# Kernel optimization log

Hardware: AMD Instinct MI355X
Metric: run time of the kernel (lower is better)

## Reference

```python
import jax, jax.numpy as jnp
import numpy as np

B, S = 2, 2048
D, H, L = 768, 12, 2
DH = D // H
WIN = 128            # one-sided sliding window
C = WIN              # query chunk size
NC = S // C
FF = 4 * D
V = 50265
SEP_ID = 2
NSEP = 16
G = NSEP + 1         # CLS + all SEP tokens are global
NCLS = 7
HID = 100
NEG = -1e9
SEP_POS = np.arange(1, NSEP + 1) * 120   # fixed [SEP] layout, same every row


def setup_inputs() -> dict:
    key = jax.random.key(0)
    ks = iter(jax.random.split(key, 32))
    def p(shape, scale=0.02):
        return scale * jax.random.normal(next(ks), shape, jnp.float32)
    input_ids = jax.random.randint(next(ks), (B, S), 10, V)
    input_ids = input_ids.at[:, SEP_POS].set(SEP_ID)
    attention_mask = jnp.ones((B, S), jnp.int32)
    return dict(
        input_ids=input_ids, attention_mask=attention_mask,
        tok_emb=p((V, D)), pos_emb=p((S, D)),
        ln_e_g=jnp.ones((D,)), ln_e_b=jnp.zeros((D,)),
        Wq=p((L, D, D)), bq=jnp.zeros((L, D)),
        Wk=p((L, D, D)), bk=jnp.zeros((L, D)),
        Wv=p((L, D, D)), bv=jnp.zeros((L, D)),
        Wo=p((L, D, D)), bo=jnp.zeros((L, D)),
        ln1_g=jnp.ones((L, D)), ln1_b=jnp.zeros((L, D)),
        W1=p((L, D, FF)), b1=jnp.zeros((L, FF)),
        W2=p((L, FF, D)), b2=jnp.zeros((L, D)),
        ln2_g=jnp.ones((L, D)), ln2_b=jnp.zeros((L, D)),
        Wh=p((2 * D, HID)), bh=jnp.zeros((HID,)),
        Wout=p((HID, NCLS)), bout=jnp.zeros((NCLS,)),
    )


def _ln(x, g, b):
    mu = jnp.mean(x, -1, keepdims=True)
    var = jnp.var(x, -1, keepdims=True)
    return (x - mu) * jax.lax.rsqrt(var + 1e-5) * g + b


def forward(input_ids, attention_mask, tok_emb, pos_emb, ln_e_g, ln_e_b,
            Wq, bq, Wk, bk, Wv, bv, Wo, bo, ln1_g, ln1_b,
            W1, b1, W2, b2, ln2_g, ln2_b, Wh, bh, Wout, bout):
    # global positions: CLS + every [SEP] (same layout in every row)
    sep_pos = jnp.nonzero(input_ids[0] == SEP_ID, size=NSEP)[0]          # [NSEP]
    glob = jnp.concatenate([jnp.zeros((1,), sep_pos.dtype), sep_pos])    # [G]

    amask = attention_mask.astype(jnp.float32)                           # [B,S]
    is_glob = jnp.zeros((S,), bool).at[glob].set(True)

    # banded (sliding-window) gather pattern, padded-coordinate indices
    idx = jnp.arange(NC)[:, None] * C + jnp.arange(3 * C)[None, :]       # [NC,3C]
    pos_k = idx - C                                                      # abs key pos
    pos_q = jnp.arange(NC)[:, None] * C + jnp.arange(C)[None, :]         # [NC,C]
    pos_k_c = jnp.clip(pos_k, 0, S - 1)
    band = jnp.abs(pos_k[:, None, :] - pos_q[:, :, None]) <= WIN         # [NC,C,3C]
    inb = (pos_k >= 0) & (pos_k < S)                                     # [NC,3C]
    # global keys are handled by the dedicated global columns -> drop from band
    band = band & (inb & ~is_glob[pos_k_c])[:, None, :]
    km = amask[:, pos_k_c] * inb                                         # [B,NC,3C]
    valid = band[None] & (km[:, :, None, :] > 0)                         # [B,NC,C,3C]
    gmask = amask[:, glob] > 0                                           # [B,G]

    x = tok_emb[input_ids] + pos_emb[None]                               # [B,S,D]
    x = _ln(x, ln_e_g, ln_e_b)

    for l in range(L):
        q = (x @ Wq[l] + bq[l]).reshape(B, S, H, DH).transpose(0, 2, 1, 3) * (DH ** -0.5)
        k = (x @ Wk[l] + bk[l]).reshape(B, S, H, DH).transpose(0, 2, 1, 3)
        v = (x @ Wv[l] + bv[l]).reshape(B, S, H, DH).transpose(0, 2, 1, 3)
        kp = jnp.pad(k, ((0, 0), (0, 0), (C, C), (0, 0)))
        vp = jnp.pad(v, ((0, 0), (0, 0), (C, C), (0, 0)))
        k3 = kp[:, :, idx]                                               # [B,H,NC,3C,DH]
        v3 = vp[:, :, idx]
        qc = q.reshape(B, H, NC, C, DH)
        s_loc = jnp.einsum('bhncd,bhnkd->bhnck', qc, k3)                 # banded scores
        s_loc = jnp.where(valid[:, None], s_loc, NEG)
        kg, vg = k[:, :, glob], v[:, :, glob]                            # [B,H,G,DH]
        s_g = jnp.einsum('bhncd,bhgd->bhncg', qc, kg)
        s_g = jnp.where(gmask[:, None, None, None, :], s_g, NEG)
        p = jax.nn.softmax(jnp.concatenate([s_loc, s_g], axis=-1), axis=-1)
        out = (jnp.einsum('bhnck,bhnkd->bhncd', p[..., :3 * C], v3)
               + jnp.einsum('bhncg,bhgd->bhncd', p[..., 3 * C:], vg))
        out = out.reshape(B, H, S, DH)
        # global query rows attend to the full sequence
        qg = q[:, :, glob]
        s_full = jnp.einsum('bhgd,bhsd->bhgs', qg, k)
        s_full = jnp.where(amask[:, None, None, :] > 0, s_full, NEG)
        out_g = jnp.einsum('bhgs,bhsd->bhgd', jax.nn.softmax(s_full, -1), v)
        out = out.at[:, :, glob, :].set(out_g)
        a = out.transpose(0, 2, 1, 3).reshape(B, S, D) @ Wo[l] + bo[l]
        x = _ln(x + a, ln1_g[l], ln1_b[l])
        h = jax.nn.gelu(x @ W1[l] + b1[l])
        x = _ln(x + h @ W2[l] + b2[l], ln2_g[l], ln2_b[l])

    # core-sentence embeddings: hstack(CLS, interior SEP embeddings)
    core = sep_pos[1:-1]                                                 # [NSEP-2]
    cls = x[:, 0, :]                                                     # [B,D]
    seps = x[:, core, :]                                                 # [B,NSEP-2,D]
    emb = jnp.concatenate([jnp.broadcast_to(cls[:, None], seps.shape), seps], -1)
    emb = emb.reshape(B * (NSEP - 2), 2 * D)
    return jax.nn.relu(emb @ Wh + bh) @ Wout + bout                      # [28, NCLS]


def reference(input_ids, attention_mask, tok_emb, pos_emb, ln_e_g, ln_e_b,
              Wq, bq, Wk, bk, Wv, bv, Wo, bo, ln1_g, ln1_b,
              W1, b1, W2, b2, ln2_g, ln2_b, Wh, bh, Wout, bout):
    return forward(input_ids, attention_mask, tok_emb, pos_emb, ln_e_g, ln_e_b,
                   Wq, bq, Wk, bk, Wv, bv, Wo, bo, ln1_g, ln1_b,
                   W1, b1, W2, b2, ln2_g, ln2_b, Wh, bh, Wout, bout)
```

## Files before the change

kernel.cpp:

```cpp
#include <hip/hip_runtime.h>
#include <hip/hip_bf16.h>
#include <math.h>

#define Sdim 2048
#define Bdim 2
#define Ddim 768
#define Hdim 12
#define DHdim 64
#define Ldim 2
#define Cdim 128
#define NCdim 16
#define FFdim 3072
#define Gdim 17
#define NSEPd 16
#define HIDd 100
#define NCLSd 7
#define SEPID 2
#define MROWS (Bdim*Sdim)
#define QKVS 2304

typedef __bf16 bf16_t;
typedef bf16_t bf16x8 __attribute__((ext_vector_type(8)));
typedef float f32x4 __attribute__((ext_vector_type(4)));
typedef ushort ushort8v __attribute__((ext_vector_type(8)));

__device__ __forceinline__ ushort f2bf(float f) {
    union { float f; unsigned u; } a; a.f = f;
    unsigned u = a.u;
    unsigned r = (u + 0x7fffu + ((u >> 16) & 1u)) >> 16;
    return (ushort)r;
}
__device__ __forceinline__ float bf2f(ushort h) {
    union { unsigned u; float f; } a; a.u = ((unsigned)h) << 16;
    return a.f;
}
__device__ __forceinline__ void gload16(const ushort* g, ushort* l) {
    __builtin_amdgcn_global_load_lds(
        (const __attribute__((address_space(1))) void*)g,
        (__attribute__((address_space(3))) void*)l, 16, 0, 0);
}

__global__ __launch_bounds__(1024) void k_findsep(const int* __restrict__ ids,
        int* __restrict__ glob, int* __restrict__ isg) {
    __shared__ unsigned long long mw[32];
    __shared__ int pfx[32];
    int t = threadIdx.x;
    int flg[2];
    #pragma unroll
    for (int pass = 0; pass < 2; ++pass) {
        int p = pass * 1024 + t;
        int f = (ids[p] == SEPID);
        flg[pass] = f;
        unsigned long long m = __ballot(f);
        if ((t & 63) == 0) mw[pass * 16 + (t >> 6)] = m;
    }
    __syncthreads();
    if (t == 0) {
        int c = 0;
        #pragma unroll
        for (int i = 0; i < 32; ++i) { pfx[i] = c; c += __popcll(mw[i]); }
        glob[0] = 0;
    }
    __syncthreads();
    #pragma unroll
    for (int pass = 0; pass < 2; ++pass) {
        int p = pass * 1024 + t;
        int w = pass * 16 + (t >> 6);
        int lane = t & 63;
        int rank = pfx[w] + __popcll(mw[w] & ((1ull << lane) - 1ull));
        int ig = 0;
        if (flg[pass] && rank < NSEPd) { glob[rank + 1] = p; ig = 1; }
        if (p == 0) ig = 1;
        isg[p] = ig;
    }
}

__global__ __launch_bounds__(256) void k_w2bt_all(
        const float* __restrict__ Wq, const float* __restrict__ Wk,
        const float* __restrict__ Wv, const float* __restrict__ Wo,
        const float* __restrict__ W1, const float* __restrict__ W2,
        ushort* __restrict__ wts) {
    const size_t WSMALL = (size_t)Ddim * Ddim;
    const size_t WBIG   = (size_t)Ddim * FFdim;
    const size_t WL     = 4 * WSMALL + 2 * WBIG;
    int bid = blockIdx.x;
    int l = bid / 1728, r = bid % 1728;
    const float* src; ushort* dst; int K, N, tile;
    ushort* base = wts + (size_t)l * WL;
    if (r < 576) {
        int w = r / 144; tile = r % 144; K = Ddim; N = Ddim;
        src = (w == 0 ? Wq : w == 1 ? Wk : w == 2 ? Wv : Wo) + (size_t)l * WSMALL;
        dst = base + (size_t)w * WSMALL;
    } else if (r < 1152) {
        tile = r - 576; K = Ddim; N = FFdim;
        src = W1 + (size_t)l * WBIG; dst = base + 4 * WSMALL;
    } else {
        tile = r - 1152; K = FFdim; N = Ddim;
        src = W2 + (size_t)l * WBIG; dst = base + 4 * WSMALL + WBIG;
    }
    int ntn = N / 64;
    int bn = (tile % ntn) * 64, bk = (tile / ntn) * 64;

    __shared__ float ts[64][65];
    int t = threadIdx.x;
    int rx = t & 63, ry = t >> 6;
    #pragma unroll
    for (int i = 0; i < 16; ++i) {
        int row = ry * 16 + i;
        ts[row][rx] = src[(size_t)(bk + row) * N + bn + rx];
    }
    __syncthreads();
    int wr = t >> 4;
    int k0 = (t & 15) * 4;
    #pragma unroll
    for (int pass = 0; pass < 4; ++pass) {
        int row = pass * 16 + wr;
        ushort4 val;
        val.x = f2bf(ts[k0 + 0][row]);
        val.y = f2bf(ts[k0 + 1][row]);
        val.z = f2bf(ts[k0 + 2][row]);
        val.w = f2bf(ts[k0 + 3][row]);
        *(ushort4*)(&dst[(size_t)(bn + row) * K + bk + k0]) = val;
    }
}

__global__ void k_biascat(const float* __restrict__ bq, const float* __restrict__ bk,
                          const float* __restrict__ bv, float* __restrict__ bqkv) {
    int l = blockIdx.x, t = threadIdx.x;
    for (int i = t; i < QKVS; i += 256) {
        float v = (i < Ddim) ? bq[l * Ddim + i]
                : (i < 2 * Ddim) ? bk[l * Ddim + i - Ddim]
                : bv[l * Ddim + i - 2 * Ddim];
        bqkv[l * QKVS + i] = v;
    }
}

__global__ __launch_bounds__(64) void k_embed(const int* __restrict__ ids,
        const float* __restrict__ tok, const float* __restrict__ pos,
        const float* __restrict__ g, const float* __restrict__ b,
        float* __restrict__ x, ushort* __restrict__ xb) {
    int row = blockIdx.x;
    int s = row & (Sdim - 1);
    long id = ids[row];
    const float4* te = (const float4*)(tok + id * (long)Ddim);
    const float4* pe = (const float4*)(pos + (long)s * Ddim);
    int t = threadIdx.x;
    float4 v[3];
    float ls = 0.f, lq = 0.f;
    #pragma unroll
    for (int i = 0; i < 3; ++i) {
        float4 a = te[i * 64 + t], p = pe[i * 64 + t];
        v[i].x = a.x + p.x; v[i].y = a.y + p.y; v[i].z = a.z + p.z; v[i].w = a.w + p.w;
        ls += v[i].x + v[i].y + v[i].z + v[i].w;
        lq += v[i].x * v[i].x + v[i].y * v[i].y + v[i].z * v[i].z + v[i].w * v[i].w;
    }
    #pragma unroll
    for (int o = 32; o; o >>= 1) { ls += __shfl_xor(ls, o, 64); lq += __shfl_xor(lq, o, 64); }
    float mu = ls / Ddim;
    float var = lq / Ddim - mu * mu;
    float rs = rsqrtf(var + 1e-5f);
    const float4* g4 = (const float4*)g;
    const float4* b4 = (const float4*)b;
    float4* xr = (float4*)(x + (long)row * Ddim);
    ushort4* xbr = (ushort4*)(xb + (long)row * Ddim);
    #pragma unroll
    for (int i = 0; i < 3; ++i) {
        float4 gg = g4[i * 64 + t], bb = b4[i * 64 + t];
        float4 o;
        o.x = (v[i].x - mu) * rs * gg.x + bb.x;
        o.y = (v[i].y - mu) * rs * gg.y + bb.y;
        o.z = (v[i].z - mu) * rs * gg.z + bb.z;
        o.w = (v[i].w - mu) * rs * gg.w + bb.w;
        xr[i * 64 + t] = o;
        ushort4 ob; ob.x = f2bf(o.x); ob.y = f2bf(o.y); ob.z = f2bf(o.z); ob.w = f2bf(o.w);
        xbr[i * 64 + t] = ob;
    }
}

__global__ __launch_bounds__(64) void k_ln_res(float* __restrict__ x,
        const float* __restrict__ a, const float* __restrict__ g,
        const float* __restrict__ b, ushort* __restrict__ xb) {
    long row = blockIdx.x;
    int t = threadIdx.x;
    const float4* xr = (const float4*)(x + row * Ddim);
    const float4* ar = (const float4*)(a + row * Ddim);
    float4 v[3];
    float ls = 0.f, lq = 0.f;
    #pragma unroll
    for (int i = 0; i < 3; ++i) {
        float4 xa = xr[i * 64 + t], aa = ar[i * 64 + t];
        v[i].x = xa.x + aa.x; v[i].y = xa.y + aa.y; v[i].z = xa.z + aa.z; v[i].w = xa.w + aa.w;
        ls += v[i].x + v[i].y + v[i].z + v[i].w;
        lq += v[i].x * v[i].x + v[i].y * v[i].y + v[i].z * v[i].z + v[i].w * v[i].w;
    }
    #pragma unroll
    for (int o = 32; o; o >>= 1) { ls += __shfl_xor(ls, o, 64); lq += __shfl_xor(lq, o, 64); }
    float mu = ls / Ddim;
    float var = lq / Ddim - mu * mu;
    float rs = rsqrtf(var + 1e-5f);
    const float4* g4 = (const float4*)g;
    const float4* b4 = (const float4*)b;
    float4* xw = (float4*)(x + row * Ddim);
    ushort4* xbr = (ushort4*)(xb + row * Ddim);
    #pragma unroll
    for (int i = 0; i < 3; ++i) {
        float4 gg = g4[i * 64 + t], bb = b4[i * 64 + t];
        float4 o;
        o.x = (v[i].x - mu) * rs * gg.x + bb.x;
        o.y = (v[i].y - mu) * rs * gg.y + bb.y;
        o.z = (v[i].z - mu) * rs * gg.z + bb.z;
        o.w = (v[i].w - mu) * rs * gg.w + bb.w;
        xw[i * 64 + t] = o;
        ushort4 ob; ob.x = f2bf(o.x); ob.y = f2bf(o.y); ob.z = f2bf(o.z); ob.w = f2bf(o.w);
        xbr[i * 64 + t] = ob;
    }
}

template<int ACT, int OUTBF16>
__global__ __launch_bounds__(256) void k_gemm_bf16(
        const ushort* __restrict__ A, const ushort* __restrict__ Wt,
        const float* __restrict__ bias, void* __restrict__ Cout,
        int M, int N, int K)
{
    __shared__ ushort As[128 * 32];
    __shared__ ushort Bs[128 * 32];
    const int t = threadIdx.x;
    const int nwg = gridDim.x * gridDim.y;
    const int wgid = blockIdx.y * gridDim.x + blockIdx.x;
    const int q8 = nwg >> 3, r8 = nwg & 7;
    const int xcd = wgid & 7, idx = wgid >> 3;
    const int swz = (xcd < r8 ? xcd * (q8 + 1) : r8 * (q8 + 1) + (xcd - r8) * q8) + idx;
    const int bm = (swz / gridDim.x) * 128;
    const int bn = (swz % gridDim.x) * 128;
    const int lane = t & 63;
    const int wv = t >> 6;
    const int wm = (wv >> 1) * 64;
    const int wn = (wv & 1) * 64;

    const int srow = t >> 2;
    const int scol = (t & 3) * 8;
    const ushort* gA0 = A + (size_t)(bm + srow) * K + scol;
    const ushort* gA1 = A + (size_t)(bm + 64 + srow) * K + scol;
    const ushort* gB0 = Wt + (size_t)(bn + srow) * K + scol;
    const ushort* gB1 = Wt + (size_t)(bn + 64 + srow) * K + scol;
    ushort* lA0 = As + t * 8;
    ushort* lA1 = As + 2048 + t * 8;
    ushort* lB0 = Bs + t * 8;
    ushort* lB1 = Bs + 2048 + t * 8;

    f32x4 acc[4][4] = {};

    const int frow = lane & 15;
    const int koff = (lane >> 4) * 8;

    for (int k0 = 0; k0 < K; k0 += 32) {
        gload16(gA0 + k0, lA0);
        gload16(gA1 + k0, lA1);
        gload16(gB0 + k0, lB0);
        gload16(gB1 + k0, lB1);
        __syncthreads();
        bf16x8 af[4], bfv[4];
        #pragma unroll
        for (int mi = 0; mi < 4; ++mi)
            af[mi] = *reinterpret_cast<const bf16x8*>(As + (wm + mi * 16 + frow) * 32 + koff);
        #pragma unroll
        for (int ni = 0; ni < 4; ++ni)
            bfv[ni] = *reinterpret_cast<const bf16x8*>(Bs + (wn + ni * 16 + frow) * 32 + koff);
        #pragma unroll
        for (int mi = 0; mi < 4; ++mi)
            #pragma unroll
            for (int ni = 0; ni < 4; ++ni)
                acc[mi][ni] = __builtin_amdgcn_mfma_f32_16x16x32_bf16(af[mi], bfv[ni], acc[mi][ni], 0, 0, 0);
        __syncthreads();
    }
    const int crow0 = (lane >> 4) * 4;
    const int ccol = lane & 15;
    #pragma unroll
    for (int mi = 0; mi < 4; ++mi) {
        #pragma unroll
        for (int ni = 0; ni < 4; ++ni) {
            int gc = bn + wn + ni * 16 + ccol;
            float bv = bias[gc];
            #pragma unroll
            for (int j = 0; j < 4; ++j) {
                int gr = bm + wm + mi * 16 + crow0 + j;
                float v = acc[mi][ni][j] + bv;
                if (ACT == 1) {
                    float y = 0.7978845608f * (v + 0.044715f * v * v * v);
                    float e = __expf(2.f * y);
                    v = v * (1.f - 1.f / (e + 1.f));
                }
                if (OUTBF16) ((ushort*)Cout)[(size_t)gr * N + gc] = f2bf(v);
                else         ((float*)Cout)[(size_t)gr * N + gc] = v;
            }
        }
    }
}

__global__ __launch_bounds__(256) void k_attn_mfma(
        const ushort* __restrict__ qkv, const int* __restrict__ isg,
        const int* __restrict__ glob, const int* __restrict__ amask,
        ushort* __restrict__ ao)
{
    const int n = blockIdx.x, h = blockIdx.y, b = blockIdx.z;
    const int t = threadIdx.x;
    const int lane = t & 63, wv = t >> 6;
    const int R0 = b * Sdim;
    const int l15 = lane & 15, l4 = lane >> 4;

    __shared__ ushort Kb[64 * 64];
    __shared__ ushort Vt[64 * 72];
    __shared__ ushort Plds[4][32 * 72];
    __shared__ float  maskLDS[448];

    for (int i = t; i < 448; i += 256) {
        int ok;
        if (i < 384) {
            int pos = n * Cdim + i - Cdim;
            ok = (pos >= 0 && pos < Sdim);
            if (ok) ok = (amask[b * Sdim + pos] != 0) && (isg[pos] == 0);
        } else {
            int g = i - 384;
            int gp = (g < Gdim) ? glob[g] : 0;
            ok = (g < Gdim) && (amask[b * Sdim + gp] != 0);
        }
        maskLDS[i] = ok ? 0.f : -1e9f;
    }

    bf16x8 qf[2][2];
    #pragma unroll
    for (int qi = 0; qi < 2; ++qi)
        #pragma unroll
        for (int kh = 0; kh < 2; ++kh)
            qf[qi][kh] = *reinterpret_cast<const bf16x8*>(
                qkv + (size_t)(R0 + n * Cdim + wv * 32 + qi * 16 + l15) * QKVS
                    + h * DHdim + kh * 32 + l4 * 8);

    f32x4 accO[2][4] = {};
    float mrow[2][4], lrow[2][4];
    #pragma unroll
    for (int qi = 0; qi < 2; ++qi)
        #pragma unroll
        for (int j = 0; j < 4; ++j) { mrow[qi][j] = -1e30f; lrow[qi][j] = 0.f; }

    const int jj = t >> 3;
    const int c16 = t & 7;

    auto ldone = [&](int j, ushort8v& kr, ushort8v& vr) {
        int pos = 0; bool ok;
        if (j < 384) { pos = n * Cdim + j - Cdim; ok = (pos >= 0 && pos < Sdim); }
        else { int g = j - 384; ok = (g < Gdim); if (ok) pos = glob[g]; }
        ushort8v z = {};
        if (ok) {
            const ushort* kp = qkv + (size_t)(R0 + pos) * QKVS + Ddim + h * DHdim + c16 * 8;
            kr = *reinterpret_cast<const ushort8v*>(kp);
            vr = *reinterpret_cast<const ushort8v*>(kp + Ddim);
        } else { kr = z; vr = z; }
    };

    ushort8v kr0, kr1, vr0, vr1, nk0 = {}, nk1 = {}, nv0 = {}, nv1 = {};
    ldone(jj, kr0, vr0);
    ldone(jj + 32, kr1, vr1);

    for (int kt = 0; kt < 7; ++kt) {
        __syncthreads();
        *reinterpret_cast<ushort8v*>(&Kb[jj * 64 + ((c16 ^ (jj & 7)) * 8)]) = kr0;
        *reinterpret_cast<ushort8v*>(&Kb[(jj + 32) * 64 + ((c16 ^ (jj & 7)) * 8)]) = kr1;
        #pragma unroll
        for (int e = 0; e < 8; ++e) {
            Vt[(c16 * 8 + e) * 72 + jj] = vr0[e];
            Vt[(c16 * 8 + e) * 72 + 32 + jj] = vr1[e];
        }
        if (kt < 6) {
            int base_j = (kt + 1) * 64 + jj;
            ldone(base_j, nk0, nv0);
            ldone(base_j + 32, nk1, nv1);
        }
        __syncthreads();

        bool active = (kt == 6) || ((kt * 64 + 63 >= wv * 32) && (kt * 64 <= wv * 32 + 287));
        if (active) {
            bf16x8 kf[4][2];
            #pragma unroll
            for (int kj = 0; kj < 4; ++kj) {
                int key = kj * 16 + l15;
                #pragma unroll
                for (int kh = 0; kh < 2; ++kh) {
                    int cc = (kh * 4 + l4) ^ (key & 7);
                    kf[kj][kh] = *reinterpret_cast<const bf16x8*>(&Kb[key * 64 + cc * 8]);
                }
            }
            float ma[4];
            #pragma unroll
            for (int kj = 0; kj < 4; ++kj) ma[kj] = maskLDS[kt * 64 + kj * 16 + l15];

            #pragma unroll
            for (int qi = 0; qi < 2; ++qi) {
                f32x4 s[4] = {};
                #pragma unroll
                for (int kj = 0; kj < 4; ++kj)
                    #pragma unroll
                    for (int kh = 0; kh < 2; ++kh)
                        s[kj] = __builtin_amdgcn_mfma_f32_16x16x32_bf16(qf[qi][kh], kf[kj][kh], s[kj], 0, 0, 0);

                float sf[4][4];
                #pragma unroll
                for (int kj = 0; kj < 4; ++kj) {
                    int key = kt * 64 + kj * 16 + l15;
                    #pragma unroll
                    for (int j = 0; j < 4; ++j) {
                        int cq = wv * 32 + qi * 16 + l4 * 4 + j;
                        float sv = s[kj][j] * 0.125f + ma[kj];
                        bool band = (key >= 384) || ((unsigned)(key - cq) <= 256u);
                        sf[kj][j] = band ? sv : sv - 1e9f;
                    }
                }
                float mnew[4], corr[4];
                #pragma unroll
                for (int j = 0; j < 4; ++j) {
                    float v = fmaxf(fmaxf(sf[0][j], sf[1][j]), fmaxf(sf[2][j], sf[3][j]));
                    v = fmaxf(v, __shfl_xor(v, 1, 64));
                    v = fmaxf(v, __shfl_xor(v, 2, 64));
                    v = fmaxf(v, __shfl_xor(v, 4, 64));
                    v = fmaxf(v, __shfl_xor(v, 8, 64));
                    mnew[j] = fmaxf(mrow[qi][j], v);
                    corr[j] = __expf(mrow[qi][j] - mnew[j]);
                    mrow[qi][j] = mnew[j];
                }
                float ps[4][4];
                #pragma unroll
                for (int kj = 0; kj < 4; ++kj)
                    #pragma unroll
                    for (int j = 0; j < 4; ++j)
                        ps[kj][j] = __expf(sf[kj][j] - mnew[j]);
                #pragma unroll
                for (int j = 0; j < 4; ++j) {
                    float r = (ps[0][j] + ps[1][j]) + (ps[2][j] + ps[3][j]);
                    r += __shfl_xor(r, 1, 64);
                    r += __shfl_xor(r, 2, 64);
                    r += __shfl_xor(r, 4, 64);
                    r += __shfl_xor(r, 8, 64);
                    lrow[qi][j] = lrow[qi][j] * corr[j] + r;
                }
                bool need = (corr[0] < 1.f) || (corr[1] < 1.f) || (corr[2] < 1.f) || (corr[3] < 1.f);
                if (__any((int)need)) {
                    #pragma unroll
                    for (int dt = 0; dt < 4; ++dt)
                        #pragma unroll
                        for (int j = 0; j < 4; ++j)
                            accO[qi][dt][j] *= corr[j];
                }
                #pragma unroll
                for (int kj = 0; kj < 4; ++kj)
                    #pragma unroll
                    for (int j = 0; j < 4; ++j)
                        Plds[wv][(qi * 16 + l4 * 4 + j) * 72 + kj * 16 + l15] = f2bf(ps[kj][j]);
            }
            #pragma unroll
            for (int qi = 0; qi < 2; ++qi) {
                #pragma unroll
                for (int ks = 0; ks < 2; ++ks) {
                    bf16x8 af = *reinterpret_cast<const bf16x8*>(
                        &Plds[wv][(qi * 16 + l15) * 72 + ks * 32 + l4 * 8]);
                    #pragma unroll
                    for (int dt = 0; dt < 4; ++dt) {
                        bf16x8 vf = *reinterpret_cast<const bf16x8*>(
                            &Vt[(dt * 16 + l15) * 72 + ks * 32 + l4 * 8]);
                        accO[qi][dt] = __builtin_amdgcn_mfma_f32_16x16x32_bf16(af, vf, accO[qi][dt], 0, 0, 0);
                    }
                }
            }
        }
        kr0 = nk0; kr1 = nk1; vr0 = nv0; vr1 = nv1;
    }

    #pragma unroll
    for (int qi = 0; qi < 2; ++qi) {
        float inv[4];
        #pragma unroll
        for (int j = 0; j < 4; ++j) inv[j] = 1.f / lrow[qi][j];
        #pragma unroll
        for (int dt = 0; dt < 4; ++dt) {
            #pragma unroll
            for (int j = 0; j < 4; ++j) {
                int crow = n * Cdim + wv * 32 + qi * 16 + l4 * 4 + j;
                ao[(size_t)(R0 + crow) * Ddim + h * DHdim + dt * 16 + l15] =
                    f2bf(accO[qi][dt][j] * inv[j]);
            }
        }
    }
}

__global__ __launch_bounds__(256) void k_attn_glob(const ushort* __restrict__ qkv,
        const int* __restrict__ glob, const int* __restrict__ amask,
        ushort* __restrict__ ao) {
    int g = blockIdx.x, h = blockIdx.y, b = blockIdx.z;
    __shared__ float sc[Sdim];
    __shared__ float qs[DHdim];
    __shared__ float redm[4], reds[4];
    __shared__ float part[32][DHdim];
    int t = threadIdx.x;
    int qr = glob[g];
    const int R0 = b * Sdim;
    if (t < DHdim)
        qs[t] = bf2f(qkv[(size_t)(R0 + qr) * QKVS + h * DHdim + t]) * 0.125f;
    __syncthreads();
    float lm = -1e30f;
    for (int s0 = t; s0 < Sdim; s0 += 256) {
        const ushort8v* kr = (const ushort8v*)(qkv + (size_t)(R0 + s0) * QKVS + Ddim + h * DHdim);
        float s = 0.f;
        #pragma unroll
        for (int cc = 0; cc < 8; ++cc) {
            ushort8v kv = kr[cc];
            #pragma unroll
            for (int e = 0; e < 8; ++e) s += qs[cc * 8 + e] * bf2f(kv[e]);
        }
        if (amask[b * Sdim + s0] == 0) s = -1e30f;
        sc[s0] = s;
        lm = fmaxf(lm, s);
    }
    #pragma unroll
    for (int o = 32; o; o >>= 1) lm = fmaxf(lm, __shfl_xor(lm, o, 64));
    if ((t & 63) == 0) redm[t >> 6] = lm;
    __syncthreads();
    float mx = fmaxf(fmaxf(redm[0], redm[1]), fmaxf(redm[2], redm[3]));
    float lsum = 0.f;
    for (int s0 = t; s0 < Sdim; s0 += 256) {
        float p = __expf(sc[s0] - mx);
        sc[s0] = p; lsum += p;
    }
    #pragma unroll
    for (int o = 32; o; o >>= 1) lsum += __shfl_xor(lsum, o, 64);
    if ((t & 63) == 0) reds[t >> 6] = lsum;
    __syncthreads();
    float l = reds[0] + reds[1] + reds[2] + reds[3];
    int chunk = t >> 3, dg = t & 7;
    float a[8] = {};
    for (int r = chunk * 64; r < chunk * 64 + 64; ++r) {
        float p = sc[r];
        ushort8v vv = *(const ushort8v*)(qkv + (size_t)(R0 + r) * QKVS + 2 * Ddim + h * DHdim + dg * 8);
        #pragma unroll
        for (int e = 0; e < 8; ++e) a[e] += p * bf2f(vv[e]);
    }
    #pragma unroll
    for (int e = 0; e < 8; ++e) part[chunk][dg * 8 + e] = a[e];
    __syncthreads();
    if (t < DHdim) {
        float o = 0.f;
        #pragma unroll
        for (int c = 0; c < 32; ++c) o += part[c][t];
        ao[(size_t)(R0 + qr) * Ddim + h * DHdim + t] = f2bf(o / l);
    }
}

__global__ __launch_bounds__(256) void k_head(const float* __restrict__ x,
        const int* __restrict__ glob, const float* __restrict__ Wh,
        const float* __restrict__ bh, const float* __restrict__ Wout,
        const float* __restrict__ bout, float* __restrict__ out) {
    int i = blockIdx.x;
    int b = i / 14, j = i % 14;
    __shared__ float emb[2 * Ddim];
    __shared__ float hp[2][128];
    __shared__ float hid[HIDd];
    int t = threadIdx.x;
    int p = glob[j + 2];
    for (int d = t; d < Ddim; d += 256) {
        emb[d] = x[(long)b * Sdim * Ddim + d];
        emb[Ddim + d] = x[((long)b * Sdim + p) * Ddim + d];
    }
    __syncthreads();
    int nn = t & 127, half = t >> 7;
    float s = 0.f;
    if (nn < HIDd) {
        int k0 = half * Ddim;
        for (int k1 = 0; k1 < Ddim; ++k1) s += emb[k0 + k1] * Wh[(k0 + k1) * HIDd + nn];
    }
    hp[half][nn] = s;
    __syncthreads();
    if (t < HIDd) hid[t] = fmaxf(hp[0][t] + hp[1][t] + bh[t], 0.f);
    __syncthreads();
    if (t < NCLSd) {
        float s2 = bout[t];
        for (int o = 0; o < HIDd; ++o) s2 += hid[o] * Wout[o * NCLSd + t];
        out[i * NCLSd + t] = s2;
    }
}

extern "C" void kernel_launch(void* const* d_in, const int* in_sizes, int n_in,
                              void* d_out, int out_size, void* d_ws, size_t ws_size,
                              hipStream_t stream) {
    const int*   ids   = (const int*)d_in[0];
    const int*   am    = (const int*)d_in[1];
    const float* tok   = (const float*)d_in[2];
    const float* pos   = (const float*)d_in[3];
    const float* lneg  = (const float*)d_in[4];
    const float* lneb  = (const float*)d_in[5];
    const float* Wq    = (const float*)d_in[6];
    const float* bq    = (const float*)d_in[7];
    const float* Wk    = (const float*)d_in[8];
    const float* bk    = (const float*)d_in[9];
    const float* Wv    = (const float*)d_in[10];
    const float* bv    = (const float*)d_in[11];
    const float* Wo    = (const float*)d_in[12];
    const float* bo    = (const float*)d_in[13];
    const float* ln1g  = (const float*)d_in[14];
    const float* ln1b  = (const float*)d_in[15];
    const float* W1    = (const float*)d_in[16];
    const float* b1    = (const float*)d_in[17];
    const float* W2    = (const float*)d_in[18];
    const float* b2    = (const float*)d_in[19];
    const float* ln2g  = (const float*)d_in[20];
    const float* ln2b  = (const float*)d_in[21];
    const float* Wh    = (const float*)d_in[22];
    const float* bh    = (const float*)d_in[23];
    const float* Wout  = (const float*)d_in[24];
    const float* bout  = (const float*)d_in[25];
    float* out = (float*)d_out;

    char* ws = (char*)d_ws;
    const size_t SZ = (size_t)MROWS * Ddim * sizeof(float);
    const size_t HB = SZ / 2;
    size_t off = 0;
    float*  x    = (float*)(ws + off);  off += SZ;
    float*  pr   = (float*)(ws + off);  off += SZ;
    ushort* xb   = (ushort*)(ws + off); off += HB;
    ushort* qkvB = (ushort*)(ws + off); off += (size_t)MROWS * QKVS * 2;
    ushort* aoB  = (ushort*)(ws + off); off += HB;
    ushort* hh   = (ushort*)(ws + off); off += (size_t)MROWS * FFdim * 2;
    const size_t WSMALL = (size_t)Ddim * Ddim;
    const size_t WBIG   = (size_t)Ddim * FFdim;
    const size_t WL     = 4 * WSMALL + 2 * WBIG;
    ushort* wts = (ushort*)(ws + off); off += WL * Ldim * 2;
    float* bqkv = (float*)(ws + off);  off += Ldim * QKVS * sizeof(float);
    int* glob = (int*)(ws + off); off += 256;
    int* isg  = (int*)(ws + off);

    k_findsep<<<1, 1024, 0, stream>>>(ids, glob, isg);
    k_biascat<<<Ldim, 256, 0, stream>>>(bq, bk, bv, bqkv);
    k_w2bt_all<<<3456, 256, 0, stream>>>(Wq, Wk, Wv, Wo, W1, W2, wts);
    k_embed<<<MROWS, 64, 0, stream>>>(ids, tok, pos, lneg, lneb, x, xb);

    dim3 g768(Ddim / 128, MROWS / 128);
    dim3 gQKV(QKVS / 128, MROWS / 128);
    dim3 gFF(FFdim / 128, MROWS / 128);
    dim3 gloc(NCdim, Hdim, Bdim);
    dim3 gglb(Gdim, Hdim, Bdim);

    for (int l = 0; l < Ldim; ++l) {
        ushort* base = wts + l * WL;
        ushort* Wqkvt = base;
        ushort* Wot = base + 3 * WSMALL;
        ushort* W1t = base + 4 * WSMALL;
        ushort* W2t = base + 4 * WSMALL + WBIG;
        k_gemm_bf16<0,1><<<gQKV, 256, 0, stream>>>(xb, Wqkvt, bqkv + l * QKVS, qkvB, MROWS, QKVS, Ddim);
        k_attn_mfma<<<gloc, 256, 0, stream>>>(qkvB, isg, glob, am, aoB);
        k_attn_glob<<<gglb, 256, 0, stream>>>(qkvB, glob, am, aoB);
        k_gemm_bf16<0,0><<<g768, 256, 0, stream>>>(aoB, Wot, bo + l * Ddim, pr, MROWS, Ddim, Ddim);
        k_ln_res<<<MROWS, 64, 0, stream>>>(x, pr, ln1g + l * Ddim, ln1b + l * Ddim, xb);
        k_gemm_bf16<1,1><<<gFF, 256, 0, stream>>>(xb, W1t, b1 + l * FFdim, hh, MROWS, FFdim, Ddim);
        k_gemm_bf16<0,0><<<g768, 256, 0, stream>>>(hh, W2t, b2 + l * Ddim, pr, MROWS, Ddim, FFdim);
        k_ln_res<<<MROWS, 64, 0, stream>>>(x, pr, ln2g + l * Ddim, ln2b + l * Ddim, xb);
    }
    k_head<<<Bdim * (NSEPd - 2), 256, 0, stream>>>(x, glob, Wh, bh, Wout, bout, out);
}
```

Baseline: 546.0 us.

## Split-K the FFN down-projection GEMM and fuse partial reduction into layernorm

The W2 GEMM (M=4096, N=768, K=3072) launched only 192 workgroups. It is now split four ways along K into 768 workgroups that write fp32 partial tiles. The new layernorm-residual kernel sums the four partials and adds the bias before normalising. The bias-concat kernel is also folded into the separator-finding kernel to save a launch. This costs extra partial-buffer traffic (three more full fp32 M×N buffers written and read) and more workspace.

```diff
diff --git a/kernel.cpp b/kernel.cpp
--- a/kernel.cpp
+++ b/kernel.cpp
@@ -18,6 +18,7 @@
 #define SEPID 2
 #define MROWS (Bdim*Sdim)
 #define QKVS 2304
+#define MNSZ (MROWS*Ddim)
 
 typedef __bf16 bf16_t;
 typedef bf16_t bf16x8 __attribute__((ext_vector_type(8)));
@@ -41,7 +42,9 @@
 }
 
 __global__ __launch_bounds__(1024) void k_findsep(const int* __restrict__ ids,
-        int* __restrict__ glob, int* __restrict__ isg) {
+        int* __restrict__ glob, int* __restrict__ isg,
+        const float* __restrict__ bq, const float* __restrict__ bk,
+        const float* __restrict__ bv, float* __restrict__ bqkv) {
     __shared__ unsigned long long mw[32];
     __shared__ int pfx[32];
     int t = threadIdx.x;
@@ -72,6 +75,13 @@
         if (flg[pass] && rank < NSEPd) { glob[rank + 1] = p; ig = 1; }
         if (p == 0) ig = 1;
         isg[p] = ig;
+    }
+    for (int idx = t; idx < Ldim * QKVS; idx += 1024) {
+        int l = idx / QKVS, i = idx % QKVS;
+        float v = (i < Ddim) ? bq[l * Ddim + i]
+                : (i < 2 * Ddim) ? bk[l * Ddim + i - Ddim]
+                : bv[l * Ddim + i - 2 * Ddim];
+        bqkv[idx] = v;
     }
 }
 
@@ -124,17 +134,6 @@
     }
 }
 
-__global__ void k_biascat(const float* __restrict__ bq, const float* __restrict__ bk,
-                          const float* __restrict__ bv, float* __restrict__ bqkv) {
-    int l = blockIdx.x, t = threadIdx.x;
-    for (int i = t; i < QKVS; i += 256) {
-        float v = (i < Ddim) ? bq[l * Ddim + i]
-                : (i < 2 * Ddim) ? bk[l * Ddim + i - Ddim]
-                : bv[l * Ddim + i - 2 * Ddim];
-        bqkv[l * QKVS + i] = v;
-    }
-}
-
 __global__ __launch_bounds__(64) void k_embed(const int* __restrict__ ids,
         const float* __restrict__ tok, const float* __restrict__ pos,
         const float* __restrict__ g, const float* __restrict__ b,
@@ -190,6 +189,54 @@
     for (int i = 0; i < 3; ++i) {
         float4 xa = xr[i * 64 + t], aa = ar[i * 64 + t];
         v[i].x = xa.x + aa.x; v[i].y = xa.y + aa.y; v[i].z = xa.z + aa.z; v[i].w = xa.w + aa.w;
+        ls += v[i].x + v[i].y + v[i].z + v[i].w;
+        lq += v[i].x * v[i].x + v[i].y * v[i].y + v[i].z * v[i].z + v[i].w * v[i].w;
+    }
+    #pragma unroll
+    for (int o = 32; o; o >>= 1) { ls += __shfl_xor(ls, o, 64); lq += __shfl_xor(lq, o, 64); }
+    float mu = ls / Ddim;
+    float var = lq / Ddim - mu * mu;
+    float rs = rsqrtf(var + 1e-5f);
+    const float4* g4 = (const float4*)g;
+    const float4* b4 = (const float4*)b;
+    float4* xw = (float4*)(x + row * Ddim);
+    ushort4* xbr = (ushort4*)(xb + row * Ddim);
+    #pragma unroll
+    for (int i = 0; i < 3; ++i) {
+        float4 gg = g4[i * 64 + t], bb = b4[i * 64 + t];
+        float4 o;
+        o.x = (v[i].x - mu) * rs * gg.x + bb.x;
+        o.y = (v[i].y - mu) * rs * gg.y + bb.y;
+        o.z = (v[i].z - mu) * rs * gg.z + bb.z;
+        o.w = (v[i].w - mu) * rs * gg.w + bb.w;
+        xw[i * 64 + t] = o;
+        ushort4 ob; ob.x = f2bf(o.x); ob.y = f2bf(o.y); ob.z = f2bf(o.z); ob.w = f2bf(o.w);
+        xbr[i * 64 + t] = ob;
+    }
+}
+
+__global__ __launch_bounds__(64) void k_ln_res4(float* __restrict__ x,
+        const float* __restrict__ pr4, const float* __restrict__ bias,
+        const float* __restrict__ g, const float* __restrict__ b,
+        ushort* __restrict__ xb) {
+    long row = blockIdx.x;
+    int t = threadIdx.x;
+    const float4* xr = (const float4*)(x + row * Ddim);
+    const float4* p0 = (const float4*)(pr4 + row * Ddim);
+    const float4* p1 = (const float4*)(pr4 + (size_t)MNSZ + row * Ddim);
+    const float4* p2 = (const float4*)(pr4 + 2 * (size_t)MNSZ + row * Ddim);
+    const float4* p3 = (const float4*)(pr4 + 3 * (size_t)MNSZ + row * Ddim);
+    const float4* bi = (const float4*)bias;
+    float4 v[3];
+    float ls = 0.f, lq = 0.f;
+    #pragma unroll
+    for (int i = 0; i < 3; ++i) {
+        int ii = i * 64 + t;
+        float4 xa = xr[ii], a0 = p0[ii], a1 = p1[ii], a2 = p2[ii], a3 = p3[ii], bb = bi[ii];
+        v[i].x = xa.x + ((a0.x + a1.x) + (a2.x + a3.x)) + bb.x;
+        v[i].y = xa.y + ((a0.y + a1.y) + (a2.y + a3.y)) + bb.y;
+        v[i].z = xa.z + ((a0.z + a1.z) + (a2.z + a3.z)) + bb.z;
+        v[i].w = xa.w + ((a0.w + a1.w) + (a2.w + a3.w)) + bb.w;
         ls += v[i].x + v[i].y + v[i].z + v[i].w;
         lq += v[i].x * v[i].x + v[i].y * v[i].y + v[i].z * v[i].z + v[i].w * v[i].w;
     }
@@ -292,6 +339,80 @@
                 }
                 if (OUTBF16) ((ushort*)Cout)[(size_t)gr * N + gc] = f2bf(v);
                 else         ((float*)Cout)[(size_t)gr * N + gc] = v;
+            }
+        }
+    }
+}
+
+__global__ __launch_bounds__(256) void k_gemm_splitk(
+        const ushort* __restrict__ A, const ushort* __restrict__ Wt,
+        float* __restrict__ Cpart, int M, int N, int K, int Kper)
+{
+    __shared__ ushort As[128 * 32];
+    __shared__ ushort Bs[128 * 32];
+    const int t = threadIdx.x;
+    const int ks = blockIdx.z;
+    const int nwg = gridDim.x * gridDim.y;
+    const int wgid = blockIdx.y * gridDim.x + blockIdx.x;
+    const int q8 = nwg >> 3, r8 = nwg & 7;
+    const int xcd = wgid & 7, idx = wgid >> 3;
+    const int swz = (xcd < r8 ? xcd * (q8 + 1) : r8 * (q8 + 1) + (xcd - r8) * q8) + idx;
+    const int bm = (swz / gridDim.x) * 128;
+    const int bn = (swz % gridDim.x) * 128;
+    const int lane = t & 63;
+    const int wv = t >> 6;
+    const int wm = (wv >> 1) * 64;
+    const int wn = (wv & 1) * 64;
+
+    const int srow = t >> 2;
+    const int scol = (t & 3) * 8;
+    const int kbase = ks * Kper;
+    const ushort* gA0 = A + (size_t)(bm + srow) * K + kbase + scol;
+    const ushort* gA1 = A + (size_t)(bm + 64 + srow) * K + kbase + scol;
+    const ushort* gB0 = Wt + (size_t)(bn + srow) * K + kbase + scol;
+    const ushort* gB1 = Wt + (size_t)(bn + 64 + srow) * K + kbase + scol;
+    ushort* lA0 = As + t * 8;
+    ushort* lA1 = As + 2048 + t * 8;
+    ushort* lB0 = Bs + t * 8;
+    ushort* lB1 = Bs + 2048 + t * 8;
+
+    f32x4 acc[4][4] = {};
+
+    const int frow = lane & 15;
+    const int koff = (lane >> 4) * 8;
+
+    for (int k0 = 0; k0 < Kper; k0 += 32) {
+        gload16(gA0 + k0, lA0);
+        gload16(gA1 + k0, lA1);
+        gload16(gB0 + k0, lB0);
+        gload16(gB1 + k0, lB1);
+        __syncthreads();
+        bf16x8 af[4], bfv[4];
+        #pragma unroll
+        for (int mi = 0; mi < 4; ++mi)
+            af[mi] = *reinterpret_cast<const bf16x8*>(As + (wm + mi * 16 + frow) * 32 + koff);
+        #pragma unroll
+        for (int ni = 0; ni < 4; ++ni)
+            bfv[ni] = *reinterpret_cast<const bf16x8*>(Bs + (wn + ni * 16 + frow) * 32 + koff);
+        #pragma unroll
+        for (int mi = 0; mi < 4; ++mi)
+            #pragma unroll
+            for (int ni = 0; ni < 4; ++ni)
+                acc[mi][ni] = __builtin_amdgcn_mfma_f32_16x16x32_bf16(af[mi], bfv[ni], acc[mi][ni], 0, 0, 0);
+        __syncthreads();
+    }
+    float* outp = Cpart + (size_t)ks * M * N;
+    const int crow0 = (lane >> 4) * 4;
+    const int ccol = lane & 15;
+    #pragma unroll
+    for (int mi = 0; mi < 4; ++mi) {
+        #pragma unroll
+        for (int ni = 0; ni < 4; ++ni) {
+            int gc = bn + wn + ni * 16 + ccol;
+            #pragma unroll
+            for (int j = 0; j < 4; ++j) {
+                int gr = bm + wm + mi * 16 + crow0 + j;
+                outp[(size_t)gr * N + gc] = acc[mi][ni][j];
             }
         }
     }
@@ -622,7 +743,7 @@
     const size_t HB = SZ / 2;
     size_t off = 0;
     float*  x    = (float*)(ws + off);  off += SZ;
-    float*  pr   = (float*)(ws + off);  off += SZ;
+    float*  pr4  = (float*)(ws + off);  off += 4 * SZ;
     ushort* xb   = (ushort*)(ws + off); off += HB;
     ushort* qkvB = (ushort*)(ws + off); off += (size_t)MROWS * QKVS * 2;
     ushort* aoB  = (ushort*)(ws + off); off += HB;
@@ -635,14 +756,14 @@
     int* glob = (int*)(ws + off); off += 256;
     int* isg  = (int*)(ws + off);
 
-    k_findsep<<<1, 1024, 0, stream>>>(ids, glob, isg);
-    k_biascat<<<Ldim, 256, 0, stream>>>(bq, bk, bv, bqkv);
+    k_findsep<<<1, 1024, 0, stream>>>(ids, glob, isg, bq, bk, bv, bqkv);
     k_w2bt_all<<<3456, 256, 0, stream>>>(Wq, Wk, Wv, Wo, W1, W2, wts);
     k_embed<<<MROWS, 64, 0, stream>>>(ids, tok, pos, lneg, lneb, x, xb);
 
     dim3 g768(Ddim / 128, MROWS / 128);
     dim3 gQKV(QKVS / 128, MROWS / 128);
     dim3 gFF(FFdim / 128, MROWS / 128);
+    dim3 gW2(Ddim / 128, MROWS / 128, 4);
     dim3 gloc(NCdim, Hdim, Bdim);
     dim3 gglb(Gdim, Hdim, Bdim);
 
@@ -655,11 +776,11 @@
         k_gemm_bf16<0,1><<<gQKV, 256, 0, stream>>>(xb, Wqkvt, bqkv + l * QKVS, qkvB, MROWS, QKVS, Ddim);
         k_attn_mfma<<<gloc, 256, 0, stream>>>(qkvB, isg, glob, am, aoB);
         k_attn_glob<<<gglb, 256, 0, stream>>>(qkvB, glob, am, aoB);
-        k_gemm_bf16<0,0><<<g768, 256, 0, stream>>>(aoB, Wot, bo + l * Ddim, pr, MROWS, Ddim, Ddim);
-        k_ln_res<<<MROWS, 64, 0, stream>>>(x, pr, ln1g + l * Ddim, ln1b + l * Ddim, xb);
+        k_gemm_bf16<0,0><<<g768, 256, 0, stream>>>(aoB, Wot, bo + l * Ddim, pr4, MROWS, Ddim, Ddim);
+        k_ln_res<<<MROWS, 64, 0, stream>>>(x, pr4, ln1g + l * Ddim, ln1b + l * Ddim, xb);
         k_gemm_bf16<1,1><<<gFF, 256, 0, stream>>>(xb, W1t, b1 + l * FFdim, hh, MROWS, FFdim, Ddim);
-        k_gemm_bf16<0,0><<<g768, 256, 0, stream>>>(hh, W2t, b2 + l * Ddim, pr, MROWS, Ddim, FFdim);
-        k_ln_res<<<MROWS, 64, 0, stream>>>(x, pr, ln2g + l * Ddim, ln2b + l * Ddim, xb);
+        k_gemm_splitk<<<gW2, 256, 0, stream>>>(hh, W2t, pr4, MROWS, Ddim, FFdim, FFdim / 4);
+        k_ln_res4<<<MROWS, 64, 0, stream>>>(x, pr4, b2 + l * Ddim, ln2g + l * Ddim, ln2b + l * Ddim, xb);
     }
     k_head<<<Bdim * (NSEPd - 2), 256, 0, stream>>>(x, glob, Wh, bh, Wout, bout, out);
 }
```

After: 486.0 us. 11.0% less time.
